# Performance work log

Measured on AMD Instinct MI355X. Metric: run time of the kernel, lower is better.

Reference implementation:

```python
import jax, jax.numpy as jnp
import numpy as np

B, C, W, H = 32, 128, 128, 128  # batch, channels, window_size, prediction_horizon
KAPPA = 10.0

def setup_inputs() -> dict:
    key = jax.random.key(0)
    k1, k2, k3, k4 = jax.random.split(key, 4)
    x_t = jax.random.normal(k1, (B, C, W), dtype=jnp.float32)
    # d are observation timestamps in [0, H), compared against ref_t = linspace(0, H, H)
    d = jax.random.uniform(k2, (B, C, W), dtype=jnp.float32) * H
    # m is an observation mask/weight in (0, 1]; avoid exact zeros for log(m)
    m = jax.random.uniform(k3, (B, C, W), dtype=jnp.float32, minval=1e-3, maxval=1.0)
    kernel = jax.random.normal(k4, (W,), dtype=jnp.float32) * 0.1
    return {"x_t": x_t, "d": d, "m": m, "kernel": kernel}

def reference(x_t, d, m, kernel):
    # ref_t: [H], matches torch.linspace(0, H, H)
    ref_t = jnp.linspace(0.0, H, H, dtype=x_t.dtype)
    # norm: [B,C,W,H] squared time differences
    norm = (d[..., None] - ref_t) ** 2
    alpha = jnp.log1p(jnp.exp(kernel))[None, None, :, None]  # softplus, [1,1,W,1]
    logm = jnp.log(m)[..., None]                             # [B,C,W,1]
    # low-intensity interpolation (softmax over window dim W)
    s = -alpha * norm + logm                                 # [B,C,W,H]
    w = jax.nn.logsumexp(s, axis=2)                          # [B,C,H]
    w1 = jnp.exp(s - w[:, :, None, :])                       # softmax weights
    y = jnp.einsum('bcwh,bcw->bch', w1, x_t)
    # high-intensity (transient) interpolation with sharper kernel kappa*alpha
    s_t = -KAPPA * alpha * norm + logm
    wt_lse = jax.nn.logsumexp(s_t, axis=2)
    w_t = jnp.exp(s_t - wt_lse[:, :, None, :])
    y_trans = jnp.einsum('bcwh,bcw->bch', w_t, x_t)
    return (y, w, y_trans)
```

## Files before the change

### kernel.cpp

```cpp
#include <hip/hip_runtime.h>
#include <hip/hip_bf16.h>

#define NB 32
#define NC 128
#define NW 128
#define NH 128
#define BCH (NB * NC * NH)

__global__ __launch_bounds__(64) void sci_kernel(
    const void* __restrict__ xp, const void* __restrict__ dp,
    const void* __restrict__ mp, const void* __restrict__ kp,
    void* __restrict__ outp)
{
    const int bid = blockIdx.x;
    const int tid = threadIdx.x;
    const int ch  = tid >> 5;
    const int ll  = tid & 31;

    __shared__ float4 tile[2][NW + 1];

    const unsigned short* du16 = (const unsigned short*)dp;
    bool is_bf16 = true;
    #pragma unroll
    for (int i = 0; i < 64; i += 2) {
        float v = __uint_as_float(((unsigned int)du16[i]) << 16);
        is_bf16 = is_bf16 && (v >= 0.0f) && (v <= 129.0f);
    }

    const float LOG2E = 1.4426950408889634f;
    #pragma unroll
    for (int j = 0; j < 4; ++j) {
        const int w = ll + 32 * j;
        const int base = (2 * bid + ch) * NW + w;
        float dv, mv, xv, kv;
        if (is_bf16) {
            dv = __bfloat162float(((const __hip_bfloat16*)dp)[base]);
            mv = __bfloat162float(((const __hip_bfloat16*)mp)[base]);
            xv = __bfloat162float(((const __hip_bfloat16*)xp)[base]);
            kv = __bfloat162float(((const __hip_bfloat16*)kp)[w]);
        } else {
            dv = ((const float*)dp)[base];
            mv = ((const float*)mp)[base];
            xv = ((const float*)xp)[base];
            kv = ((const float*)kp)[w];
        }
        float A2  = log1pf(__expf(kv)) * LOG2E;
        float sA2 = sqrtf(A2);
        tile[ch][w] = make_float4(sA2, sA2 * dv, mv, mv * xv);
    }
    __syncthreads();

    float rh[4];
    #pragma unroll
    for (int j = 0; j < 4; ++j) rh[j] = (float)(ll + 32 * j) * (128.0f / 127.0f);

    float mn[4] = {3.0e38f, 3.0e38f, 3.0e38f, 3.0e38f};
    #pragma unroll 8
    for (int w = 0; w < NW; ++w) {
        float2 q = *(const float2*)&tile[ch][w];
        #pragma unroll
        for (int j = 0; j < 4; ++j) {
            float t = __builtin_fmaf(-q.x, rh[j], q.y);
            mn[j] = fminf(mn[j], t * t);
        }
    }

    float s1[4] = {0.f, 0.f, 0.f, 0.f}, a1[4] = {0.f, 0.f, 0.f, 0.f};
    float s2[4] = {0.f, 0.f, 0.f, 0.f}, a2[4] = {0.f, 0.f, 0.f, 0.f};
    #pragma unroll 2
    for (int w = 0; w < NW; ++w) {
        float4 q = tile[ch][w];
        #pragma unroll
        for (int j = 0; j < 4; ++j) {
            float t  = __builtin_fmaf(-q.x, rh[j], q.y);
            float v  = __builtin_fmaf(-t, t, mn[j]);
            float g1 = __builtin_amdgcn_exp2f(v);
            float sq = g1 * g1;
            float p4 = sq * sq;
            float p8 = p4 * p4;
            float g2 = p8 * sq;
            s1[j] = __builtin_fmaf(q.z, g1, s1[j]);
            a1[j] = __builtin_fmaf(q.w, g1, a1[j]);
            s2[j] = __builtin_fmaf(q.z, g2, s2[j]);
            a2[j] = __builtin_fmaf(q.w, g2, a2[j]);
        }
    }

    const float LN2 = 0.6931471805599453f;
    const int obase = (2 * bid + ch) * NH + ll;
    #pragma unroll
    for (int j = 0; j < 4; ++j) {
        float y  = a1[j] * __builtin_amdgcn_rcpf(s1[j]);
        float wv = (__builtin_amdgcn_logf(s1[j]) - mn[j]) * LN2;
        float yt = a2[j] * __builtin_amdgcn_rcpf(s2[j]);
        const int o = obase + 32 * j;
        if (is_bf16) {
            __hip_bfloat16* o16 = (__hip_bfloat16*)outp;
            o16[o]           = __float2bfloat16(y);
            o16[BCH + o]     = __float2bfloat16(wv);
            o16[2 * BCH + o] = __float2bfloat16(yt);
        } else {
            float* o32 = (float*)outp;
            o32[o]           = y;
            o32[BCH + o]     = wv;
            o32[2 * BCH + o] = yt;
        }
    }
}

extern "C" void kernel_launch(void* const* d_in, const int* in_sizes, int n_in,
                              void* d_out, int out_size, void* d_ws, size_t ws_size,
                              hipStream_t stream) {
    const void* x_t = d_in[0];
    const void* d   = d_in[1];
    const void* m   = d_in[2];
    const void* k   = d_in[3];
    dim3 grid(NB * NC / 2);
    dim3 block(64);
    hipLaunchKernelGGL(sci_kernel, grid, block, 0, stream, x_t, d, m, k, d_out);
}
```

Baseline: 89.73 us.

## Split the window reduction across half-wavefronts, one (b,c) row per block

Each 64-thread block now handles a single (b,c) row instead of two. The two half-wavefronts each reduce over half of the window dimension, and the partial minima and sums are combined with cross-lane shuffles. This doubles the grid size and halves the serial loop length per thread to expose more parallelism and hide latency. The cost is extra shuffle and reduction work, and half the lanes sit idle during the output stores.

```diff
diff --git a/kernel.cpp b/kernel.cpp
--- a/kernel.cpp
+++ b/kernel.cpp
@@ -12,12 +12,12 @@
     const void* __restrict__ mp, const void* __restrict__ kp,
     void* __restrict__ outp)
 {
-    const int bid = blockIdx.x;
+    const int bc  = blockIdx.x;
     const int tid = threadIdx.x;
-    const int ch  = tid >> 5;
     const int ll  = tid & 31;
+    const int wbase = (tid >> 5) * 64;
 
-    __shared__ float4 tile[2][NW + 1];
+    __shared__ float4 tile[NW];
 
     const unsigned short* du16 = (const unsigned short*)dp;
     bool is_bf16 = true;
@@ -29,9 +29,9 @@
 
     const float LOG2E = 1.4426950408889634f;
     #pragma unroll
-    for (int j = 0; j < 4; ++j) {
-        const int w = ll + 32 * j;
-        const int base = (2 * bid + ch) * NW + w;
+    for (int j = 0; j < 2; ++j) {
+        const int w = tid + 64 * j;
+        const int base = bc * NW + w;
         float dv, mv, xv, kv;
         if (is_bf16) {
             dv = __bfloat162float(((const __hip_bfloat16*)dp)[base]);
@@ -46,7 +46,7 @@
         }
         float A2  = log1pf(__expf(kv)) * LOG2E;
         float sA2 = sqrtf(A2);
-        tile[ch][w] = make_float4(sA2, sA2 * dv, mv, mv * xv);
+        tile[w] = make_float4(sA2, sA2 * dv, mv, mv * xv);
     }
     __syncthreads();
 
@@ -54,22 +54,29 @@
     #pragma unroll
     for (int j = 0; j < 4; ++j) rh[j] = (float)(ll + 32 * j) * (128.0f / 127.0f);
 
-    float mn[4] = {3.0e38f, 3.0e38f, 3.0e38f, 3.0e38f};
+    float mna[4] = {3.0e38f, 3.0e38f, 3.0e38f, 3.0e38f};
     #pragma unroll 8
-    for (int w = 0; w < NW; ++w) {
-        float2 q = *(const float2*)&tile[ch][w];
+    for (int i = 0; i < 64; ++i) {
+        float2 q = *(const float2*)&tile[wbase + i];
         #pragma unroll
         for (int j = 0; j < 4; ++j) {
             float t = __builtin_fmaf(-q.x, rh[j], q.y);
-            mn[j] = fminf(mn[j], t * t);
+            mna[j] = fminf(mna[j], fabsf(t));
         }
+    }
+    float mn[4];
+    #pragma unroll
+    for (int j = 0; j < 4; ++j) {
+        float o = __shfl_xor(mna[j], 32);
+        float a = fminf(mna[j], o);
+        mn[j] = a * a;
     }
 
     float s1[4] = {0.f, 0.f, 0.f, 0.f}, a1[4] = {0.f, 0.f, 0.f, 0.f};
     float s2[4] = {0.f, 0.f, 0.f, 0.f}, a2[4] = {0.f, 0.f, 0.f, 0.f};
     #pragma unroll 2
-    for (int w = 0; w < NW; ++w) {
-        float4 q = tile[ch][w];
+    for (int i = 0; i < 64; ++i) {
+        float4 q = tile[wbase + i];
         #pragma unroll
         for (int j = 0; j < 4; ++j) {
             float t  = __builtin_fmaf(-q.x, rh[j], q.y);
@@ -86,24 +93,34 @@
         }
     }
 
-    const float LN2 = 0.6931471805599453f;
-    const int obase = (2 * bid + ch) * NH + ll;
     #pragma unroll
     for (int j = 0; j < 4; ++j) {
-        float y  = a1[j] * __builtin_amdgcn_rcpf(s1[j]);
-        float wv = (__builtin_amdgcn_logf(s1[j]) - mn[j]) * LN2;
-        float yt = a2[j] * __builtin_amdgcn_rcpf(s2[j]);
-        const int o = obase + 32 * j;
-        if (is_bf16) {
-            __hip_bfloat16* o16 = (__hip_bfloat16*)outp;
-            o16[o]           = __float2bfloat16(y);
-            o16[BCH + o]     = __float2bfloat16(wv);
-            o16[2 * BCH + o] = __float2bfloat16(yt);
-        } else {
-            float* o32 = (float*)outp;
-            o32[o]           = y;
-            o32[BCH + o]     = wv;
-            o32[2 * BCH + o] = yt;
+        s1[j] += __shfl_xor(s1[j], 32);
+        a1[j] += __shfl_xor(a1[j], 32);
+        s2[j] += __shfl_xor(s2[j], 32);
+        a2[j] += __shfl_xor(a2[j], 32);
+    }
+
+    if (tid < 32) {
+        const float LN2 = 0.6931471805599453f;
+        const int obase = bc * NH + ll;
+        #pragma unroll
+        for (int j = 0; j < 4; ++j) {
+            float y  = a1[j] * __builtin_amdgcn_rcpf(s1[j]);
+            float wv = (__builtin_amdgcn_logf(s1[j]) - mn[j]) * LN2;
+            float yt = a2[j] * __builtin_amdgcn_rcpf(s2[j]);
+            const int o = obase + 32 * j;
+            if (is_bf16) {
+                __hip_bfloat16* o16 = (__hip_bfloat16*)outp;
+                o16[o]           = __float2bfloat16(y);
+                o16[BCH + o]     = __float2bfloat16(wv);
+                o16[2 * BCH + o] = __float2bfloat16(yt);
+            } else {
+                float* o32 = (float*)outp;
+                o32[o]           = y;
+                o32[BCH + o]     = wv;
+                o32[2 * BCH + o] = yt;
+            }
         }
     }
 }
@@ -115,7 +132,7 @@
     const void* d   = d_in[1];
     const void* m   = d_in[2];
     const void* k   = d_in[3];
-    dim3 grid(NB * NC / 2);
+    dim3 grid(NB * NC);
     dim3 block(64);
     hipLaunchKernelGGL(sci_kernel, grid, block, 0, stream, x_t, d, m, k, d_out);
 }
```

Result: faster. 83.10 us (-7.4%).
